# Kernel tuning notes

Hardware: AMD Instinct MI355X
Metric: run time of the kernel (lower is better)

The kernel has to match this reference:

```python
import jax, jax.numpy as jnp
import numpy as np

V, D, H, L, S = 50257, 1024, 16, 4, 4096
DH = D // H  # 64
DF = 4 * D   # 4096


def _layernorm(x, g, b, eps=1e-5):
    m = jnp.mean(x, axis=-1, keepdims=True)
    v = jnp.mean(jnp.square(x - m), axis=-1, keepdims=True)
    return (x - m) / jnp.sqrt(v + eps) * g + b


def _pos_encoding(s, d):
    # standard sinusoidal positional encoding [s, d]
    pos = jnp.arange(s, dtype=jnp.float32)[:, None]
    i = jnp.arange(d // 2, dtype=jnp.float32)[None, :]
    ang = pos * jnp.exp(-(2.0 * i / d) * jnp.log(10000.0))
    return jnp.concatenate([jnp.sin(ang), jnp.cos(ang)], axis=-1)


def setup_inputs() -> dict:
    key = jax.random.key(0)
    ks = jax.random.split(key, 8)
    s = 0.02
    return {
        "tokens": jax.random.randint(ks[0], (S,), 0, V),
        "emb": jax.random.normal(ks[1], (V, D), jnp.float32) * s,
        "Wq": jax.random.normal(ks[2], (L, H, D, DH), jnp.float32) * s,
        "bq": jnp.zeros((L, H, DH), jnp.float32),
        "Wk": jax.random.normal(ks[3], (L, H, D, DH), jnp.float32) * s,
        "bk": jnp.zeros((L, H, DH), jnp.float32),
        "Wv": jax.random.normal(ks[4], (L, H, D, DH), jnp.float32) * s,
        "bv": jnp.zeros((L, H, DH), jnp.float32),
        "ln1_g": jnp.ones((L, D), jnp.float32),
        "ln1_b": jnp.zeros((L, D), jnp.float32),
        "W1": jax.random.normal(ks[5], (L, D, DF), jnp.float32) * s,
        "b1": jnp.zeros((L, DF), jnp.float32),
        "W2": jax.random.normal(ks[6], (L, DF, D), jnp.float32) * s,
        "b2": jnp.zeros((L, D), jnp.float32),
        "ln2_g": jnp.ones((L, D), jnp.float32),
        "ln2_b": jnp.zeros((L, D), jnp.float32),
        "Wout": jax.random.normal(ks[7], (D, V), jnp.float32) * s,
        "bout": jnp.zeros((V,), jnp.float32),
    }


def reference(tokens, emb, Wq, bq, Wk, bk, Wv, bv, ln1_g, ln1_b,
              W1, b1, W2, b2, ln2_g, ln2_b, Wout, bout):
    x = emb[tokens] + _pos_encoding(S, D)          # [S, D]
    scale = 1.0 / jnp.sqrt(jnp.float32(DH))
    for l in range(L):
        # per-head projections: [H, S, DH]
        q = jnp.einsum("sd,hde->hse", x, Wq[l]) + bq[l][:, None, :]
        k = jnp.einsum("sd,hde->hse", x, Wk[l]) + bk[l][:, None, :]
        v = jnp.einsum("sd,hde->hse", x, Wv[l]) + bv[l][:, None, :]
        att = jax.nn.softmax(jnp.einsum("hse,hte->hst", q, k) * scale, axis=-1)
        y = jnp.einsum("hst,hte->hse", att, v)      # [H, S, DH]
        y = jnp.transpose(y, (1, 0, 2)).reshape(S, D)  # concat heads
        x = _layernorm(x + y, ln1_g[l], ln1_b[l])
        y = jnp.maximum(x @ W1[l] + b1[l], 0.0) @ W2[l] + b2[l]  # FFN
        x = _layernorm(x + y, ln2_g[l], ln2_b[l])
    logits = x @ Wout + bout                        # [S, V]
    return jax.nn.softmax(logits, axis=-1)
```

## Files before the change

### kernel.cpp

```cpp
#include <hip/hip_runtime.h>
#include <math.h>

#define S_LEN  4096
#define DMODEL 1024
#define NHEAD  16
#define DHEAD  64
#define DFF    4096
#define NLAYER 4
#define VOCAB  50257
#define NCBP   400

typedef unsigned short ushort_t;
typedef __attribute__((ext_vector_type(8))) __bf16 bf16x8;
typedef __attribute__((ext_vector_type(4))) float f32x4;

static __device__ __forceinline__ ushort_t f2bf(float f) {
  union { float f; unsigned u; } x; x.f = f;
  unsigned r = x.u + 0x7fffu + ((x.u >> 16) & 1u);
  return (ushort_t)(r >> 16);
}
static __device__ __forceinline__ float bf2f(ushort_t h) {
  union { unsigned u; float f; } x; x.u = ((unsigned)h) << 16;
  return x.f;
}
static __device__ __forceinline__ float exp2fast(float x) {
  return __builtin_amdgcn_exp2f(x);
}

#define GLOAD_LDS16(gp, lp) \
  __builtin_amdgcn_global_load_lds((const __attribute__((address_space(1))) void*)(gp), \
                                   (__attribute__((address_space(3))) void*)(lp), 16, 0, 0)

#define QSCALE 0.18033688011112042f

__global__ __launch_bounds__(256) void embed_kernel(
    const int* __restrict__ tokens, const float* __restrict__ emb,
    float* __restrict__ x, ushort_t* __restrict__ xh)
{
  int s = blockIdx.x;
  int tok = tokens[s];
  int d0 = threadIdx.x * 4;
  const double lf = 0.01798894603901598653;
  float4 ev = *(const float4*)(emb + (size_t)tok * DMODEL + d0);
  float o[4]; float evr[4] = {ev.x, ev.y, ev.z, ev.w};
  #pragma unroll
  for (int j = 0; j < 4; ++j) {
    int d = d0 + j;
    int i = (d < 512) ? d : d - 512;
    double ang = (double)s * exp(-lf * (double)i);
    float pe = (d < 512) ? (float)sin(ang) : (float)cos(ang);
    o[j] = evr[j] + pe;
  }
  *(float4*)(x + (size_t)s * DMODEL + d0) = make_float4(o[0], o[1], o[2], o[3]);
  ushort_t hv[4];
  #pragma unroll
  for (int j = 0; j < 4; ++j) hv[j] = f2bf(o[j]);
  *(ushort4*)(xh + (size_t)s * DMODEL + d0) = make_ushort4(hv[0], hv[1], hv[2], hv[3]);
}

__global__ __launch_bounds__(256)
void transpose_split(const float* __restrict__ in, ushort_t* __restrict__ oh,
                     ushort_t* __restrict__ ol,
                     long in_zstr, long out_zoff, long in_z2str, long out_z2off,
                     int zdiv, int in_rstride, int Kout, int Nvalid)
{
  __shared__ float tile[64][65];
  int z1 = blockIdx.z % zdiv, z2 = blockIdx.z / zdiv;
  long ioff = (long)z1 * in_zstr + (long)z2 * in_z2str;
  long ooff = (long)z1 * out_zoff + (long)z2 * out_z2off;
  const float* inz = in + ioff;
  ushort_t* ohz = oh + ooff;
  ushort_t* olz = ol + ooff;
  int k0 = blockIdx.x * 64, n0 = blockIdx.y * 64;
  int t = threadIdx.x;
  #pragma unroll
  for (int i = 0; i < 4; ++i) {
    int idx = t + i * 256;
    int kk = idx >> 4, c4 = idx & 15;
    #pragma unroll
    for (int j = 0; j < 4; ++j) {
      int n = n0 + c4 * 4 + j;
      float v = (n < Nvalid) ? inz[(long)(k0 + kk) * in_rstride + n] : 0.f;
      tile[c4 * 4 + j][kk] = v;
    }
  }
  __syncthreads();
  #pragma unroll
  for (int i = 0; i < 4; ++i) {
    int idx = t + i * 256;
    int nn = idx >> 4, k4 = idx & 15;
    ushort_t hv[4], lv[4];
    #pragma unroll
    for (int j = 0; j < 4; ++j) {
      float v = tile[nn][k4 * 4 + j];
      hv[j] = f2bf(v);
      lv[j] = f2bf(v - bf2f(hv[j]));
    }
    long ob = (long)(n0 + nn) * Kout + k0 + k4 * 4;
    *(ushort4*)(ohz + ob) = make_ushort4(hv[0], hv[1], hv[2], hv[3]);
    *(ushort4*)(olz + ob) = make_ushort4(lv[0], lv[1], lv[2], lv[3]);
  }
}

__global__ __launch_bounds__(256)
void transpose_h(const float* __restrict__ in, ushort_t* __restrict__ oh,
                 int in_rstride, int Kout, int Nvalid)
{
  __shared__ float tile[64][65];
  int k0 = blockIdx.x * 64, n0 = blockIdx.y * 64;
  int t = threadIdx.x;
  #pragma unroll
  for (int i = 0; i < 4; ++i) {
    int idx = t + i * 256;
    int kk = idx >> 4, c4 = idx & 15;
    #pragma unroll
    for (int j = 0; j < 4; ++j) {
      int n = n0 + c4 * 4 + j;
      float v = (n < Nvalid) ? in[(long)(k0 + kk) * in_rstride + n] : 0.f;
      tile[c4 * 4 + j][kk] = v;
    }
  }
  __syncthreads();
  #pragma unroll
  for (int i = 0; i < 4; ++i) {
    int idx = t + i * 256;
    int nn = idx >> 4, k4 = idx & 15;
    ushort_t hv[4];
    #pragma unroll
    for (int j = 0; j < 4; ++j) hv[j] = f2bf(tile[nn][k4 * 4 + j]);
    long ob = (long)(n0 + nn) * Kout + k0 + k4 * 4;
    *(ushort4*)(oh + ob) = make_ushort4(hv[0], hv[1], hv[2], hv[3]);
  }
}

__global__ __launch_bounds__(256)
void transpose_v(const ushort_t* __restrict__ vb, ushort_t* __restrict__ vt)
{
  __shared__ ushort_t tile[64][72];
  int h = blockIdx.y, s0 = blockIdx.x * 64;
  int t = threadIdx.x;
  const ushort_t* src = vb + ((size_t)h * S_LEN + s0) * 64;
  #pragma unroll
  for (int i = 0; i < 4; ++i) {
    int idx = t + i * 256;
    int row = idx >> 4, c4 = idx & 15;
    *(ushort4*)&tile[row][c4 * 4] = *(const ushort4*)(src + (size_t)row * 64 + c4 * 4);
  }
  __syncthreads();
  ushort_t* dst = vt + (size_t)h * DHEAD * S_LEN + s0;
  #pragma unroll
  for (int i = 0; i < 4; ++i) {
    int idx = t + i * 256;
    int e = idx >> 4, s4 = idx & 15;
    ushort4 o = make_ushort4(tile[s4*4+0][e], tile[s4*4+1][e],
                             tile[s4*4+2][e], tile[s4*4+3][e]);
    *(ushort4*)(dst + (size_t)e * S_LEN + s4 * 4) = o;
  }
}

__global__ __launch_bounds__(256)
void concat3_kernel(const float* __restrict__ a, const float* __restrict__ b,
                    const float* __restrict__ c, float* __restrict__ o,
                    int n, long lstrA, long lstrO)
{
  int i = blockIdx.x * 256 + threadIdx.x;
  long l = blockIdx.y;
  if (i < n) {
    o[l * lstrO + i]         = a[l * lstrA + i];
    o[l * lstrO + n + i]     = b[l * lstrA + i];
    o[l * lstrO + 2 * n + i] = c[l * lstrA + i];
  }
}

template<int EPI, bool RELU>
__global__ __launch_bounds__(512, 2)
void gemm8p(const ushort_t* __restrict__ Ah,
            const ushort_t* __restrict__ Bh, const ushort_t* __restrict__ Bl,
            const float* __restrict__ bias, float* __restrict__ C,
            ushort_t* __restrict__ O0, ushort_t* __restrict__ O1,
            ushort_t* __restrict__ O2, ushort_t* __restrict__ O4,
            int K, int ldk, long ldc, long czStride)
{
  constexpr int BUFSTR = 3 * 8192;
  constexpr int OBH = 8192, OBL = 16384;
  __shared__ ushort_t lds[2 * BUFSTR];

  const int t = threadIdx.x;
  const int l = t & 63;
  const int w = t >> 6;
  const int wr = w >> 2;
  const int wc = w & 3;
  const int lrow = l & 15;
  const int lk = (l >> 4) * 8;
  const int l8 = l * 8;
  const long m0 = (long)blockIdx.x * 256;
  const long n0 = (long)blockIdx.y * 256;
  const long kz = (long)blockIdx.z * K;

  const ushort_t *agp[2], *bgp[2], *blgp[2];
  int dst[2];
  #pragma unroll
  for (int i = 0; i < 2; ++i) {
    int s = i * 8 + w;
    dst[i] = s * 512 + l8;
    agp[i]  = Ah + (m0 + s * 16 + lrow) * (long)ldk + kz + lk;
    bgp[i]  = Bh + (n0 + s * 16 + lrow) * (long)ldk + kz + lk;
    blgp[i] = Bl + (n0 + s * 16 + lrow) * (long)ldk + kz + lk;
  }

  f32x4 acc[8][4];
  #pragma unroll
  for (int m = 0; m < 8; ++m)
    #pragma unroll
    for (int n = 0; n < 4; ++n) acc[m][n] = (f32x4)0.f;

  GLOAD_LDS16(agp[0],  &lds[dst[0]]);
  GLOAD_LDS16(agp[1],  &lds[dst[1]]);
  GLOAD_LDS16(bgp[0],  &lds[OBH + dst[0]]);
  GLOAD_LDS16(bgp[1],  &lds[OBH + dst[1]]);
  GLOAD_LDS16(blgp[0], &lds[OBL + dst[0]]);
  GLOAD_LDS16(blgp[1], &lds[OBL + dst[1]]);

  const int nk = K >> 5;
  int cur = 0;
  for (int kt = 0; kt < nk; ++kt) {
    const int knx = (kt + 1 < nk) ? (kt + 1) * 32 : 0;
    ushort_t* cb = &lds[cur * BUFSTR];
    ushort_t* nb = &lds[(cur ^ 1) * BUFSTR];
    bf16x8 af[8], bhf[4], blf[4];

    asm volatile("s_waitcnt vmcnt(2)" ::: "memory");
    __builtin_amdgcn_sched_barrier(0);
    __builtin_amdgcn_s_barrier();
    __builtin_amdgcn_sched_barrier(0);
    #pragma unroll
    for (int m = 0; m < 8; ++m)
      af[m] = *(const bf16x8*)&cb[(wr * 8 + m) * 512 + l8];
    #pragma unroll
    for (int n = 0; n < 4; ++n)
      bhf[n] = *(const bf16x8*)&cb[OBH + (wc * 4 + n) * 512 + l8];
    GLOAD_LDS16(agp[0] + knx, &nb[dst[0]]);
    GLOAD_LDS16(agp[1] + knx, &nb[dst[1]]);
    GLOAD_LDS16(bgp[0] + knx, &nb[OBH + dst[0]]);
    __builtin_amdgcn_s_setprio(1);
    #pragma unroll
    for (int m = 0; m < 8; ++m)
      #pragma unroll
      for (int n = 0; n < 4; ++n)
        acc[m][n] = __builtin_amdgcn_mfma_f32_16x16x32_bf16(af[m], bhf[n], acc[m][n], 0, 0, 0);
    __builtin_amdgcn_s_setprio(0);
    __builtin_amdgcn_sched_barrier(0);

    asm volatile("s_waitcnt vmcnt(3)" ::: "memory");
    __builtin_amdgcn_sched_barrier(0);
    __builtin_amdgcn_s_barrier();
    __builtin_amdgcn_sched_barrier(0);
    #pragma unroll
    for (int n = 0; n < 4; ++n)
      blf[n] = *(const bf16x8*)&cb[OBL + (wc * 4 + n) * 512 + l8];
    GLOAD_LDS16(bgp[1] + knx,  &nb[OBH + dst[1]]);
    GLOAD_LDS16(blgp[0] + knx, &nb[OBL + dst[0]]);
    GLOAD_LDS16(blgp[1] + knx, &nb[OBL + dst[1]]);
    __builtin_amdgcn_s_setprio(1);
    #pragma unroll
    for (int m = 0; m < 8; ++m)
      #pragma unroll
      for (int n = 0; n < 4; ++n)
        acc[m][n] = __builtin_amdgcn_mfma_f32_16x16x32_bf16(af[m], blf[n], acc[m][n], 0, 0, 0);
    __builtin_amdgcn_s_setprio(0);
    __builtin_amdgcn_sched_barrier(0);
    cur ^= 1;
  }
  asm volatile("s_waitcnt vmcnt(0)" ::: "memory");

  if constexpr (EPI == 2) {
    #pragma unroll
    for (int n = 0; n < 4; ++n) {
      long col = n0 + wc * 64 + n * 16 + lrow;
      float bv = bias[col];
      #pragma unroll
      for (int m = 0; m < 8; ++m) {
        #pragma unroll
        for (int r = 0; r < 4; ++r) {
          long row = m0 + wr * 128 + m * 16 + (l >> 4) * 4 + r;
          float v = acc[m][n][r] + bv;
          int c = (int)col;
          if (c < 1024) {
            int hh = c >> 6, e = c & 63;
            float qv = v * QSCALE;
            ushort_t hi = f2bf(qv);
            size_t a = ((size_t)hh * S_LEN + row) * 64 + e;
            O0[a] = hi; O1[a] = f2bf(qv - bf2f(hi));
          } else if (c < 2048) {
            int cc = c - 1024;
            int hh = cc >> 6, e = cc & 63;
            size_t a = ((size_t)hh * S_LEN + row) * 64 + e;
            O2[a] = f2bf(v);
          } else {
            int cc = c - 2048;
            int hh = cc >> 6, e = cc & 63;
            size_t a = ((size_t)hh * S_LEN + row) * 64 + e;
            O4[a] = f2bf(v);
          }
        }
      }
    }
  } else if constexpr (EPI == 1) {
    #pragma unroll
    for (int n = 0; n < 4; ++n) {
      long col = n0 + wc * 64 + n * 16 + lrow;
      float bv = bias[col];
      #pragma unroll
      for (int m = 0; m < 8; ++m) {
        #pragma unroll
        for (int r = 0; r < 4; ++r) {
          long row = m0 + wr * 128 + m * 16 + (l >> 4) * 4 + r;
          float v = acc[m][n][r] + bv;
          if (RELU) v = fmaxf(v, 0.f);
          O0[row * ldc + col] = f2bf(v);
        }
      }
    }
  } else {
    float* Cz = C + (long)blockIdx.z * czStride;
    #pragma unroll
    for (int n = 0; n < 4; ++n) {
      long col = n0 + wc * 64 + n * 16 + lrow;
      #pragma unroll
      for (int m = 0; m < 8; ++m) {
        #pragma unroll
        for (int r = 0; r < 4; ++r) {
          long row = m0 + wr * 128 + m * 16 + (l >> 4) * 4 + r;
          Cz[row * ldc + col] = acc[m][n][r];
        }
      }
    }
  }
}

template<bool BOUND>
__global__ __launch_bounds__(512, 2)
void gemm1p(const ushort_t* __restrict__ Ah, const ushort_t* __restrict__ Bh,
            const float* __restrict__ bias, float* __restrict__ C,
            int K, int ldk, long ldc, int Nlimit,
            float* __restrict__ Ppart, int cbbase)
{
  constexpr int OB = 8192;
  constexpr int BUFSTR = 16384;
  __shared__ ushort_t lds[2 * BUFSTR];
  __shared__ float psum[1024];

  const int t = threadIdx.x;
  const int l = t & 63;
  const int w = t >> 6;
  const int wr = w >> 2;
  const int wc = w & 3;
  const int lrow = l & 15;
  const int lk = (l >> 4) * 8;
  const int l8 = l * 8;
  const long m0 = (long)blockIdx.x * 256;
  const long n0 = (long)blockIdx.y * 256;

  const ushort_t *agp[2], *bgp[2];
  int dst[2];
  #pragma unroll
  for (int i = 0; i < 2; ++i) {
    int s = i * 8 + w;
    dst[i] = s * 512 + l8;
    agp[i] = Ah + (m0 + s * 16 + lrow) * (long)ldk + lk;
    bgp[i] = Bh + (n0 + s * 16 + lrow) * (long)ldk + lk;
  }

  f32x4 acc[8][4];
  #pragma unroll
  for (int m = 0; m < 8; ++m)
    #pragma unroll
    for (int n = 0; n < 4; ++n) acc[m][n] = (f32x4)0.f;

  GLOAD_LDS16(agp[0], &lds[dst[0]]);
  GLOAD_LDS16(agp[1], &lds[dst[1]]);
  GLOAD_LDS16(bgp[0], &lds[OB + dst[0]]);
  GLOAD_LDS16(bgp[1], &lds[OB + dst[1]]);
  GLOAD_LDS16(agp[0] + 32, &lds[BUFSTR + dst[0]]);
  GLOAD_LDS16(agp[1] + 32, &lds[BUFSTR + dst[1]]);
  GLOAD_LDS16(bgp[0] + 32, &lds[BUFSTR + OB + dst[0]]);
  GLOAD_LDS16(bgp[1] + 32, &lds[BUFSTR + OB + dst[1]]);

  const int nk = K >> 5;
  int cur = 0;
  for (int kt = 0; kt < nk; ++kt) {
    ushort_t* cb = &lds[cur * BUFSTR];
    bf16x8 af[8], bhf[4];

    asm volatile("s_waitcnt vmcnt(4)" ::: "memory");
    __builtin_amdgcn_sched_barrier(0);
    __builtin_amdgcn_s_barrier();
    __builtin_amdgcn_sched_barrier(0);
    #pragma unroll
    for (int m = 0; m < 8; ++m)
      af[m] = *(const bf16x8*)&cb[(wr * 8 + m) * 512 + l8];
    #pragma unroll
    for (int n = 0; n < 4; ++n)
      bhf[n] = *(const bf16x8*)&cb[OB + (wc * 4 + n) * 512 + l8];
    __builtin_amdgcn_sched_barrier(0);
    asm volatile("s_waitcnt lgkmcnt(0)" ::: "memory");
    __builtin_amdgcn_sched_barrier(0);
    __builtin_amdgcn_s_barrier();
    __builtin_amdgcn_sched_barrier(0);
    const int knx2 = (kt + 2 < nk) ? (kt + 2) * 32 : 0;
    GLOAD_LDS16(agp[0] + knx2, &cb[dst[0]]);
    GLOAD_LDS16(agp[1] + knx2, &cb[dst[1]]);
    GLOAD_LDS16(bgp[0] + knx2, &cb[OB + dst[0]]);
    GLOAD_LDS16(bgp[1] + knx2, &cb[OB + dst[1]]);
    __builtin_amdgcn_s_setprio(1);
    #pragma unroll
    for (int m = 0; m < 8; ++m)
      #pragma unroll
      for (int n = 0; n < 4; ++n)
        acc[m][n] = __builtin_amdgcn_mfma_f32_16x16x32_bf16(af[m], bhf[n], acc[m][n], 0, 0, 0);
    __builtin_amdgcn_s_setprio(0);
    __builtin_amdgcn_sched_barrier(0);
    cur ^= 1;
  }
  asm volatile("s_waitcnt vmcnt(0)" ::: "memory");

  float smr[8][4];
  #pragma unroll
  for (int m = 0; m < 8; ++m)
    #pragma unroll
    for (int r = 0; r < 4; ++r) smr[m][r] = 0.f;
  #pragma unroll
  for (int n = 0; n < 4; ++n) {
    long col = n0 + wc * 64 + n * 16 + lrow;
    bool cok = (!BOUND) || (col < (long)Nlimit);
    float bv = cok ? bias[col] : 0.f;
    #pragma unroll
    for (int m = 0; m < 8; ++m) {
      #pragma unroll
      for (int r = 0; r < 4; ++r) {
        long row = m0 + wr * 128 + m * 16 + (l >> 4) * 4 + r;
        float e = cok ? __expf(acc[m][n][r] + bv) : 0.f;
        if (cok) C[row * ldc + col] = e;
        smr[m][r] += e;
      }
    }
  }
  #pragma unroll
  for (int m = 0; m < 8; ++m) {
    #pragma unroll
    for (int r = 0; r < 4; ++r) {
      float s = smr[m][r];
      s += __shfl_xor(s, 1);
      s += __shfl_xor(s, 2);
      s += __shfl_xor(s, 4);
      s += __shfl_xor(s, 8);
      if (lrow == 0)
        psum[wc * 256 + wr * 128 + m * 16 + (l >> 4) * 4 + r] = s;
    }
  }
  __syncthreads();
  if (t < 256) {
    float s = psum[t] + psum[256 + t] + psum[512 + t] + psum[768 + t];
    Ppart[(m0 + t) * NCBP + cbbase + blockIdx.y] = s;
  }
}

__global__ __launch_bounds__(256)
void attn_mfma(const ushort_t* __restrict__ qh, const ushort_t* __restrict__ ql,
               const ushort_t* __restrict__ kh, const ushort_t* __restrict__ vt,
               float* __restrict__ y)
{
  __shared__ ushort_t lds[16384];

  const int t = threadIdx.x, l = t & 63, w = t >> 6;
  const int lrow = l & 15, lhi = l >> 4;
  const int h = blockIdx.y;
  const int bw = blockIdx.x * 128 + w * 32;
  const size_t hS = (size_t)h * S_LEN * DHEAD;
  const size_t hV = (size_t)h * DHEAD * S_LEN;
  const int pb = 8192 + w * 2048;

  bf16x8 qhf[2][2], qlf[2][2];
  #pragma unroll
  for (int m = 0; m < 2; ++m)
    #pragma unroll
    for (int ks = 0; ks < 2; ++ks) {
      size_t a = hS + (size_t)(bw + m * 16 + lrow) * 64 + ks * 32 + lhi * 8;
      qhf[m][ks] = *(const bf16x8*)(qh + a);
      qlf[m][ks] = *(const bf16x8*)(ql + a);
    }

  f32x4 acc[2][4];
  #pragma unroll
  for (int m = 0; m < 2; ++m)
    #pragma unroll
    for (int n = 0; n < 4; ++n) acc[m][n] = (f32x4)0.f;
  float mrow[8], lsum[8];
  #pragma unroll
  for (int i = 0; i < 8; ++i) { mrow[i] = -1e30f; lsum[i] = 0.f; }

  for (int kt = 0; kt < S_LEN; kt += 64) {
    __syncthreads();
    #pragma unroll
    for (int i = 0; i < 2; ++i) {
      int s = i * 4 + w;
      size_t krow = (size_t)(kt + (s >> 1) * 16 + lrow);
      int koff = (s & 1) * 32 + lhi * 8;
      GLOAD_LDS16(kh + hS + krow * 64 + koff, &lds[s * 512 + l * 8]);
      size_t erow = (size_t)((s >> 1) * 16 + lrow);
      int toff = kt + (s & 1) * 32 + lhi * 8;
      GLOAD_LDS16(vt + hV + erow * S_LEN + toff, &lds[4096 + s * 512 + l * 8]);
    }
    __syncthreads();

    f32x4 sacc[2][4];
    #pragma unroll
    for (int m = 0; m < 2; ++m)
      #pragma unroll
      for (int n = 0; n < 4; ++n) sacc[m][n] = (f32x4)0.f;
    #pragma unroll
    for (int ks = 0; ks < 2; ++ks) {
      bf16x8 bh_[4];
      #pragma unroll
      for (int n = 0; n < 4; ++n)
        bh_[n] = *(const bf16x8*)&lds[(n * 2 + ks) * 512 + l * 8];
      #pragma unroll
      for (int m = 0; m < 2; ++m)
        #pragma unroll
        for (int n = 0; n < 4; ++n) {
          sacc[m][n] = __builtin_amdgcn_mfma_f32_16x16x32_bf16(qhf[m][ks], bh_[n], sacc[m][n], 0, 0, 0);
          sacc[m][n] = __builtin_amdgcn_mfma_f32_16x16x32_bf16(qlf[m][ks], bh_[n], sacc[m][n], 0, 0, 0);
        }
    }

    float tmv[2][4];
    bool up = false;
    #pragma unroll
    for (int m = 0; m < 2; ++m) {
      #pragma unroll
      for (int r = 0; r < 4; ++r) {
        float tm = fmaxf(fmaxf(sacc[m][0][r], sacc[m][1][r]),
                         fmaxf(sacc[m][2][r], sacc[m][3][r]));
        tm = fmaxf(tm, __shfl_xor(tm, 1));
        tm = fmaxf(tm, __shfl_xor(tm, 2));
        tm = fmaxf(tm, __shfl_xor(tm, 4));
        tm = fmaxf(tm, __shfl_xor(tm, 8));
        tmv[m][r] = tm;
        up = up || (tm > mrow[m * 4 + r]);
      }
    }
    if (__ballot(up) != 0ULL) {
      #pragma unroll
      for (int m = 0; m < 2; ++m) {
        #pragma unroll
        for (int r = 0; r < 4; ++r) {
          const int idx = m * 4 + r;
          float mn = fmaxf(mrow[idx], tmv[m][r]);
          float al = exp2fast(mrow[idx] - mn);
          mrow[idx] = mn;
          lsum[idx] *= al;
          #pragma unroll
          for (int n = 0; n < 4; ++n) acc[m][n][r] *= al;
        }
      }
    }
    #pragma unroll
    for (int m = 0; m < 2; ++m) {
      #pragma unroll
      for (int r = 0; r < 4; ++r) {
        const int idx = m * 4 + r;
        float rs = 0.f;
        #pragma unroll
        for (int n = 0; n < 4; ++n) {
          float p = exp2fast(sacc[m][n][r] - mrow[idx]);
          rs += p;
          int pa = pb + ((m * 2 + (n >> 1)) << 9) + (((n & 1) * 2 + (lrow >> 3)) << 7)
                   + ((lhi * 4 + r) << 3) + (l & 7);
          pa ^= (lrow >> 3) << 3;
          lds[pa] = f2bf(p);
        }
        rs += __shfl_xor(rs, 1);
        rs += __shfl_xor(rs, 2);
        rs += __shfl_xor(rs, 4);
        rs += __shfl_xor(rs, 8);
        lsum[idx] += rs;
      }
    }

    #pragma unroll
    for (int ks = 0; ks < 2; ++ks) {
      bf16x8 pa_[2];
      #pragma unroll
      for (int m = 0; m < 2; ++m) {
        int ra = pb + ((m * 2 + ks) << 9) + (l << 3);
        ra ^= ((l >> 4) & 1) << 3;
        pa_[m] = *(const bf16x8*)&lds[ra];
      }
      #pragma unroll
      for (int n = 0; n < 4; ++n) {
        bf16x8 vf = *(const bf16x8*)&lds[4096 + (n * 2 + ks) * 512 + l * 8];
        #pragma unroll
        for (int m = 0; m < 2; ++m)
          acc[m][n] = __builtin_amdgcn_mfma_f32_16x16x32_bf16(pa_[m], vf, acc[m][n], 0, 0, 0);
      }
    }
  }

  #pragma unroll
  for (int m = 0; m < 2; ++m) {
    #pragma unroll
    for (int r = 0; r < 4; ++r) {
      float inv = 1.0f / lsum[m * 4 + r];
      int row = bw + m * 16 + lhi * 4 + r;
      #pragma unroll
      for (int n = 0; n < 4; ++n)
        y[(size_t)row * DMODEL + h * 64 + n * 16 + lrow] = acc[m][n][r] * inv;
    }
  }
}

__device__ __forceinline__ float block_sum256(float v, float* sm)
{
  #pragma unroll
  for (int off = 32; off >= 1; off >>= 1) v += __shfl_xor(v, off);
  int w = threadIdx.x >> 6;
  if ((threadIdx.x & 63) == 0) sm[w] = v;
  __syncthreads();
  v = sm[0] + sm[1] + sm[2] + sm[3];
  __syncthreads();
  return v;
}

__global__ __launch_bounds__(256)
void resid_ln_kernel(float* __restrict__ x, const float* __restrict__ y,
                     const float* __restrict__ g, const float* __restrict__ b,
                     ushort_t* __restrict__ xh)
{
  __shared__ float sm[4];
  int row = blockIdx.x, t = threadIdx.x;
  float4 xv = *(const float4*)(x + (size_t)row * DMODEL + t * 4);
  float4 yv = *(const float4*)(y + (size_t)row * DMODEL + t * 4);
  float a0 = xv.x + yv.x, a1 = xv.y + yv.y, a2 = xv.z + yv.z, a3 = xv.w + yv.w;
  float s = block_sum256(a0 + a1 + a2 + a3, sm);
  float mean = s * (1.0f / DMODEL);
  float d0 = a0 - mean, d1 = a1 - mean, d2 = a2 - mean, d3 = a3 - mean;
  float vs = block_sum256(d0*d0 + d1*d1 + d2*d2 + d3*d3, sm);
  float inv = rsqrtf(vs * (1.0f / DMODEL) + 1e-5f);
  float4 gv = *(const float4*)(g + t * 4);
  float4 bv = *(const float4*)(b + t * 4);
  float o[4];
  o[0] = d0 * inv * gv.x + bv.x;
  o[1] = d1 * inv * gv.y + bv.y;
  o[2] = d2 * inv * gv.z + bv.z;
  o[3] = d3 * inv * gv.w + bv.w;
  *(float4*)(x + (size_t)row * DMODEL + t * 4) = make_float4(o[0], o[1], o[2], o[3]);
  ushort_t hv[4];
  #pragma unroll
  for (int j = 0; j < 4; ++j) hv[j] = f2bf(o[j]);
  *(ushort4*)(xh + (size_t)row * DMODEL + t * 4) = make_ushort4(hv[0], hv[1], hv[2], hv[3]);
}

__global__ __launch_bounds__(256)
void resid_ln_red(float* __restrict__ x, const float* __restrict__ parts,
                  long pstride, const float* __restrict__ bias,
                  const float* __restrict__ g, const float* __restrict__ b,
                  ushort_t* __restrict__ xh)
{
  __shared__ float sm[4];
  int row = blockIdx.x, t = threadIdx.x;
  size_t base = (size_t)row * DMODEL + t * 4;
  float4 xv = *(const float4*)(x + base);
  float4 bb = *(const float4*)(bias + t * 4);
  float a0 = xv.x + bb.x, a1 = xv.y + bb.y, a2 = xv.z + bb.z, a3 = xv.w + bb.w;
  #pragma unroll
  for (int z = 0; z < 4; ++z) {
    float4 pv = *(const float4*)(parts + (size_t)z * pstride + base);
    a0 += pv.x; a1 += pv.y; a2 += pv.z; a3 += pv.w;
  }
  float s = block_sum256(a0 + a1 + a2 + a3, sm);
  float mean = s * (1.0f / DMODEL);
  float d0 = a0 - mean, d1 = a1 - mean, d2 = a2 - mean, d3 = a3 - mean;
  float vs = block_sum256(d0*d0 + d1*d1 + d2*d2 + d3*d3, sm);
  float inv = rsqrtf(vs * (1.0f / DMODEL) + 1e-5f);
  float4 gv = *(const float4*)(g + t * 4);
  float4 bv = *(const float4*)(b + t * 4);
  float o[4];
  o[0] = d0 * inv * gv.x + bv.x;
  o[1] = d1 * inv * gv.y + bv.y;
  o[2] = d2 * inv * gv.z + bv.z;
  o[3] = d3 * inv * gv.w + bv.w;
  *(float4*)(x + base) = make_float4(o[0], o[1], o[2], o[3]);
  ushort_t hv[4];
  #pragma unroll
  for (int j = 0; j < 4; ++j) hv[j] = f2bf(o[j]);
  *(ushort4*)(xh + base) = make_ushort4(hv[0], hv[1], hv[2], hv[3]);
}

__global__ __launch_bounds__(256)
void scale_softmax(float* __restrict__ out, const float* __restrict__ partials,
                   int ncb)
{
  __shared__ float sm[4];
  int row = blockIdx.x, t = threadIdx.x;
  float s = 0.f;
  for (int cb = t; cb < ncb; cb += 256) s += partials[(size_t)row * NCBP + cb];
  s = block_sum256(s, sm);
  float inv = 1.0f / s;
  float* p = out + (size_t)row * VOCAB;
  int head = (int)((((uintptr_t)16 - ((uintptr_t)p & 15)) & 15) >> 2);
  if (t < head) p[t] *= inv;
  int nvec = (VOCAB - head) >> 2;
  float4* pv = (float4*)(p + head);
  for (int i = t; i < nvec; i += 256) {
    float4 v = pv[i];
    v.x *= inv; v.y *= inv; v.z *= inv; v.w *= inv;
    pv[i] = v;
  }
  int done = head + nvec * 4;
  if (t < VOCAB - done) p[done + t] *= inv;
}

extern "C" void kernel_launch(void* const* d_in, const int* in_sizes, int n_in,
                              void* d_out, int out_size, void* d_ws, size_t ws_size,
                              hipStream_t stream)
{
  const int*   tokens = (const int*)  d_in[0];
  const float* emb    = (const float*)d_in[1];
  const float* Wq     = (const float*)d_in[2];
  const float* bq     = (const float*)d_in[3];
  const float* Wk     = (const float*)d_in[4];
  const float* bk     = (const float*)d_in[5];
  const float* Wv     = (const float*)d_in[6];
  const float* bv     = (const float*)d_in[7];
  const float* ln1g   = (const float*)d_in[8];
  const float* ln1b   = (const float*)d_in[9];
  const float* W1     = (const float*)d_in[10];
  const float* b1     = (const float*)d_in[11];
  const float* W2     = (const float*)d_in[12];
  const float* b2     = (const float*)d_in[13];
  const float* ln2g   = (const float*)d_in[14];
  const float* ln2b   = (const float*)d_in[15];
  const float* Wout   = (const float*)d_in[16];
  const float* bout   = (const float*)d_in[17];

  char* wsb = (char*)d_ws;
  ushort_t* xh     = (ushort_t*)(wsb);
  ushort_t* stripH = (ushort_t*)(wsb + ((size_t)8  << 20));
  float*    partials = (float*)(wsb + ((size_t)24 << 20));

  char* ob = (char*)d_out;
  float*    x     = (float*)(ob);
  float*    yb    = (float*)(ob + ((size_t)16  << 20));
  ushort_t* qh    = (ushort_t*)(ob + ((size_t)32  << 20));
  ushort_t* ql    = (ushort_t*)(ob + ((size_t)40  << 20));
  ushort_t* kh    = (ushort_t*)(ob + ((size_t)48  << 20));
  ushort_t* vb16  = (ushort_t*)(ob + ((size_t)56  << 20));
  ushort_t* vt    = (ushort_t*)(ob + ((size_t)64  << 20));
  ushort_t* h1h   = (ushort_t*)(ob + ((size_t)72  << 20));
  float*    fparts= (float*)(ob + ((size_t)104 << 20));
  ushort_t* wqkvhA= (ushort_t*)(ob + ((size_t)168 << 20));
  ushort_t* wqkvlA= (ushort_t*)(ob + ((size_t)192 << 20));
  ushort_t* w1hA  = (ushort_t*)(ob + ((size_t)216 << 20));
  ushort_t* w1lA  = (ushort_t*)(ob + ((size_t)248 << 20));
  ushort_t* w2hA  = (ushort_t*)(ob + ((size_t)280 << 20));
  ushort_t* w2lA  = (ushort_t*)(ob + ((size_t)312 << 20));
  float*    bqkvA = (float*)(ob + ((size_t)344 << 20));
  float*    outf  = (float*)d_out;

  const long WQKV_L = 3072L * 1024;
  const long WFF_L  = 4096L * 1024;

  embed_kernel<<<S_LEN, 256, 0, stream>>>(tokens, emb, x, xh);

  transpose_split<<<dim3(16, 1, 64), 256, 0, stream>>>(
      Wq, wqkvhA, wqkvlA,
      (long)DMODEL * DHEAD, (long)DHEAD * DMODEL,
      (long)NHEAD * DMODEL * DHEAD, WQKV_L,
      16, DHEAD, DMODEL, DHEAD);
  transpose_split<<<dim3(16, 1, 64), 256, 0, stream>>>(
      Wk, wqkvhA + 1024 * 1024, wqkvlA + 1024 * 1024,
      (long)DMODEL * DHEAD, (long)DHEAD * DMODEL,
      (long)NHEAD * DMODEL * DHEAD, WQKV_L,
      16, DHEAD, DMODEL, DHEAD);
  transpose_split<<<dim3(16, 1, 64), 256, 0, stream>>>(
      Wv, wqkvhA + 2048 * 1024, wqkvlA + 2048 * 1024,
      (long)DMODEL * DHEAD, (long)DHEAD * DMODEL,
      (long)NHEAD * DMODEL * DHEAD, WQKV_L,
      16, DHEAD, DMODEL, DHEAD);
  transpose_split<<<dim3(16, 64, 4), 256, 0, stream>>>(
      W1, w1hA, w1lA, 0, 0,
      (long)DMODEL * DFF, WFF_L, 1, DFF, DMODEL, DFF);
  transpose_split<<<dim3(64, 16, 4), 256, 0, stream>>>(
      W2, w2hA, w2lA, 0, 0,
      (long)DFF * DMODEL, WFF_L, 1, DMODEL, DFF, DMODEL);
  concat3_kernel<<<dim3(4, NLAYER), 256, 0, stream>>>(
      bq, bk, bv, bqkvA, 1024, 1024, 3072);

  for (int l = 0; l < NLAYER; ++l) {
    const ushort_t* wqh = wqkvhA + (long)l * WQKV_L;
    const ushort_t* wql = wqkvlA + (long)l * WQKV_L;
    const ushort_t* w1h = w1hA + (long)l * WFF_L;
    const ushort_t* w1l = w1lA + (long)l * WFF_L;
    const ushort_t* w2h = w2hA + (long)l * WFF_L;
    const ushort_t* w2l = w2lA + (long)l * WFF_L;

    gemm8p<2, false><<<dim3(16, 12), 512, 0, stream>>>(
        xh, wqh, wql, bqkvA + (long)l * 3072, nullptr,
        qh, ql, kh, vb16, 1024, 1024, 0, 0);
    transpose_v<<<dim3(64, 16), 256, 0, stream>>>(vb16, vt);

    attn_mfma<<<dim3(32, 16), 256, 0, stream>>>(qh, ql, kh, vt, yb);

    resid_ln_kernel<<<S_LEN, 256, 0, stream>>>(x, yb,
        ln1g + (size_t)l * DMODEL, ln1b + (size_t)l * DMODEL, xh);

    gemm8p<1, true><<<dim3(16, 16), 512, 0, stream>>>(
        xh, w1h, w1l, b1 + (long)l * DFF, nullptr,
        h1h, nullptr, nullptr, nullptr, 1024, 1024, 4096, 0);
    gemm8p<0, false><<<dim3(16, 4, 4), 512, 0, stream>>>(
        h1h, w2h, w2l, nullptr, fparts,
        nullptr, nullptr, nullptr, nullptr,
        1024, 4096, 1024, (long)S_LEN * DMODEL);
    resid_ln_red<<<S_LEN, 256, 0, stream>>>(x, fparts, (long)S_LEN * DMODEL,
        b2 + (long)l * DMODEL,
        ln2g + (size_t)l * DMODEL, ln2b + (size_t)l * DMODEL, xh);
  }

  const int SW = 4096;
  for (int is = 0; is < 12; ++is) {
    int n0 = is * SW;
    transpose_h<<<dim3(16, 64, 1), 256, 0, stream>>>(
        Wout + n0, stripH, VOCAB, DMODEL, SW);
    gemm1p<false><<<dim3(16, 16), 512, 0, stream>>>(
        xh, stripH, bout + n0, outf + n0,
        1024, 1024, VOCAB, SW, partials, is * 16);
  }
  {
    int n0 = 12 * SW;
    int ncols = VOCAB - n0;
    int nt64 = (ncols + 63) / 64;
    int nb256 = (ncols + 255) / 256;
    transpose_h<<<dim3(16, nt64, 1), 256, 0, stream>>>(
        Wout + n0, stripH, VOCAB, DMODEL, ncols);
    gemm1p<true><<<dim3(16, nb256), 512, 0, stream>>>(
        xh, stripH, bout + n0, outf + n0,
        1024, 1024, VOCAB, ncols, partials, 12 * 16);
  }
  const int ncb = (VOCAB + 255) / 256;
  scale_softmax<<<S_LEN, 256, 0, stream>>>(outf, partials, ncb);
}
```

Before: 3.820 ms.

## Double-buffer attention K/V loads, fuse V transpose into QKV epilogue, single-shot vocab GEMM

The attention kernel now double-buffers its K/V tiles in LDS, prefetching the next tile while the current one is computed, with a single barrier per iteration. The QKV GEMM epilogue writes V directly in transposed layout, which removes the separate transpose_v kernel and one round trip through memory. When the workspace is large enough, the output projection transposes all of Wout once and runs one GEMM over the whole vocabulary instead of twelve strip launches. The costs are more LDS per block, strided scattered stores in the V epilogue, and a dependence on workspace size.

```diff
diff --git a/kernel.cpp b/kernel.cpp
--- a/kernel.cpp
+++ b/kernel.cpp
@@ -130,31 +130,6 @@
     for (int j = 0; j < 4; ++j) hv[j] = f2bf(tile[nn][k4 * 4 + j]);
     long ob = (long)(n0 + nn) * Kout + k0 + k4 * 4;
     *(ushort4*)(oh + ob) = make_ushort4(hv[0], hv[1], hv[2], hv[3]);
-  }
-}
-
-__global__ __launch_bounds__(256)
-void transpose_v(const ushort_t* __restrict__ vb, ushort_t* __restrict__ vt)
-{
-  __shared__ ushort_t tile[64][72];
-  int h = blockIdx.y, s0 = blockIdx.x * 64;
-  int t = threadIdx.x;
-  const ushort_t* src = vb + ((size_t)h * S_LEN + s0) * 64;
-  #pragma unroll
-  for (int i = 0; i < 4; ++i) {
-    int idx = t + i * 256;
-    int row = idx >> 4, c4 = idx & 15;
-    *(ushort4*)&tile[row][c4 * 4] = *(const ushort4*)(src + (size_t)row * 64 + c4 * 4);
-  }
-  __syncthreads();
-  ushort_t* dst = vt + (size_t)h * DHEAD * S_LEN + s0;
-  #pragma unroll
-  for (int i = 0; i < 4; ++i) {
-    int idx = t + i * 256;
-    int e = idx >> 4, s4 = idx & 15;
-    ushort4 o = make_ushort4(tile[s4*4+0][e], tile[s4*4+1][e],
-                             tile[s4*4+2][e], tile[s4*4+3][e]);
-    *(ushort4*)(dst + (size_t)e * S_LEN + s4 * 4) = o;
   }
 }
 
@@ -299,7 +274,7 @@
           } else {
             int cc = c - 2048;
             int hh = cc >> 6, e = cc & 63;
-            size_t a = ((size_t)hh * S_LEN + row) * 64 + e;
+            size_t a = ((size_t)hh * DHEAD + e) * S_LEN + row;
             O4[a] = f2bf(v);
           }
         }
@@ -470,7 +445,7 @@
                const ushort_t* __restrict__ kh, const ushort_t* __restrict__ vt,
                float* __restrict__ y)
 {
-  __shared__ ushort_t lds[16384];
+  __shared__ ushort_t lds[24576];
 
   const int t = threadIdx.x, l = t & 63, w = t >> 6;
   const int lrow = l & 15, lhi = l >> 4;
@@ -478,7 +453,7 @@
   const int bw = blockIdx.x * 128 + w * 32;
   const size_t hS = (size_t)h * S_LEN * DHEAD;
   const size_t hV = (size_t)h * DHEAD * S_LEN;
-  const int pb = 8192 + w * 2048;
+  const int pb = 16384 + w * 2048;
 
   bf16x8 qhf[2][2], qlf[2][2];
   #pragma unroll
@@ -499,19 +474,37 @@
   #pragma unroll
   for (int i = 0; i < 8; ++i) { mrow[i] = -1e30f; lsum[i] = 0.f; }
 
+  #pragma unroll
+  for (int i = 0; i < 2; ++i) {
+    int s = i * 4 + w;
+    size_t krow = (size_t)((s >> 1) * 16 + lrow);
+    int koff = (s & 1) * 32 + lhi * 8;
+    GLOAD_LDS16(kh + hS + krow * 64 + koff, &lds[s * 512 + l * 8]);
+    int toff = (s & 1) * 32 + lhi * 8;
+    GLOAD_LDS16(vt + hV + krow * S_LEN + toff, &lds[4096 + s * 512 + l * 8]);
+  }
+
+  int cur = 0;
   for (int kt = 0; kt < S_LEN; kt += 64) {
-    __syncthreads();
-    #pragma unroll
-    for (int i = 0; i < 2; ++i) {
-      int s = i * 4 + w;
-      size_t krow = (size_t)(kt + (s >> 1) * 16 + lrow);
-      int koff = (s & 1) * 32 + lhi * 8;
-      GLOAD_LDS16(kh + hS + krow * 64 + koff, &lds[s * 512 + l * 8]);
-      size_t erow = (size_t)((s >> 1) * 16 + lrow);
-      int toff = kt + (s & 1) * 32 + lhi * 8;
-      GLOAD_LDS16(vt + hV + erow * S_LEN + toff, &lds[4096 + s * 512 + l * 8]);
-    }
-    __syncthreads();
+    asm volatile("s_waitcnt vmcnt(0)" ::: "memory");
+    __builtin_amdgcn_sched_barrier(0);
+    __builtin_amdgcn_s_barrier();
+    __builtin_amdgcn_sched_barrier(0);
+    ushort_t* cb = &lds[cur * 8192];
+    if (kt + 64 < S_LEN) {
+      ushort_t* nb = &lds[(cur ^ 1) * 8192];
+      int kn = kt + 64;
+      #pragma unroll
+      for (int i = 0; i < 2; ++i) {
+        int s = i * 4 + w;
+        size_t krow = (size_t)(kn + (s >> 1) * 16 + lrow);
+        int koff = (s & 1) * 32 + lhi * 8;
+        GLOAD_LDS16(kh + hS + krow * 64 + koff, &nb[s * 512 + l * 8]);
+        size_t erow = (size_t)((s >> 1) * 16 + lrow);
+        int toff = kn + (s & 1) * 32 + lhi * 8;
+        GLOAD_LDS16(vt + hV + erow * S_LEN + toff, &nb[4096 + s * 512 + l * 8]);
+      }
+    }
 
     f32x4 sacc[2][4];
     #pragma unroll
@@ -523,7 +516,7 @@
       bf16x8 bh_[4];
       #pragma unroll
       for (int n = 0; n < 4; ++n)
-        bh_[n] = *(const bf16x8*)&lds[(n * 2 + ks) * 512 + l * 8];
+        bh_[n] = *(const bf16x8*)&cb[(n * 2 + ks) * 512 + l * 8];
       #pragma unroll
       for (int m = 0; m < 2; ++m)
         #pragma unroll
@@ -598,12 +591,13 @@
       }
       #pragma unroll
       for (int n = 0; n < 4; ++n) {
-        bf16x8 vf = *(const bf16x8*)&lds[4096 + (n * 2 + ks) * 512 + l * 8];
+        bf16x8 vf = *(const bf16x8*)&cb[4096 + (n * 2 + ks) * 512 + l * 8];
         #pragma unroll
         for (int m = 0; m < 2; ++m)
           acc[m][n] = __builtin_amdgcn_mfma_f32_16x16x32_bf16(pa_[m], vf, acc[m][n], 0, 0, 0);
       }
     }
+    cur ^= 1;
   }
 
   #pragma unroll
@@ -747,6 +741,8 @@
   ushort_t* xh     = (ushort_t*)(wsb);
   ushort_t* stripH = (ushort_t*)(wsb + ((size_t)8  << 20));
   float*    partials = (float*)(wsb + ((size_t)24 << 20));
+  ushort_t* woutT  = (ushort_t*)(wsb + ((size_t)32 << 20));
+  const bool bigws = ws_size >= ((size_t)137 << 20);
 
   char* ob = (char*)d_out;
   float*    x     = (float*)(ob);
@@ -754,17 +750,16 @@
   ushort_t* qh    = (ushort_t*)(ob + ((size_t)32  << 20));
   ushort_t* ql    = (ushort_t*)(ob + ((size_t)40  << 20));
   ushort_t* kh    = (ushort_t*)(ob + ((size_t)48  << 20));
-  ushort_t* vb16  = (ushort_t*)(ob + ((size_t)56  << 20));
-  ushort_t* vt    = (ushort_t*)(ob + ((size_t)64  << 20));
-  ushort_t* h1h   = (ushort_t*)(ob + ((size_t)72  << 20));
-  float*    fparts= (float*)(ob + ((size_t)104 << 20));
-  ushort_t* wqkvhA= (ushort_t*)(ob + ((size_t)168 << 20));
-  ushort_t* wqkvlA= (ushort_t*)(ob + ((size_t)192 << 20));
-  ushort_t* w1hA  = (ushort_t*)(ob + ((size_t)216 << 20));
-  ushort_t* w1lA  = (ushort_t*)(ob + ((size_t)248 << 20));
-  ushort_t* w2hA  = (ushort_t*)(ob + ((size_t)280 << 20));
-  ushort_t* w2lA  = (ushort_t*)(ob + ((size_t)312 << 20));
-  float*    bqkvA = (float*)(ob + ((size_t)344 << 20));
+  ushort_t* vt    = (ushort_t*)(ob + ((size_t)56  << 20));
+  ushort_t* h1h   = (ushort_t*)(ob + ((size_t)64  << 20));
+  float*    fparts= (float*)(ob + ((size_t)96  << 20));
+  ushort_t* wqkvhA= (ushort_t*)(ob + ((size_t)160 << 20));
+  ushort_t* wqkvlA= (ushort_t*)(ob + ((size_t)184 << 20));
+  ushort_t* w1hA  = (ushort_t*)(ob + ((size_t)208 << 20));
+  ushort_t* w1lA  = (ushort_t*)(ob + ((size_t)240 << 20));
+  ushort_t* w2hA  = (ushort_t*)(ob + ((size_t)272 << 20));
+  ushort_t* w2lA  = (ushort_t*)(ob + ((size_t)304 << 20));
+  float*    bqkvA = (float*)(ob + ((size_t)336 << 20));
   float*    outf  = (float*)d_out;
 
   const long WQKV_L = 3072L * 1024;
@@ -806,8 +801,7 @@
 
     gemm8p<2, false><<<dim3(16, 12), 512, 0, stream>>>(
         xh, wqh, wql, bqkvA + (long)l * 3072, nullptr,
-        qh, ql, kh, vb16, 1024, 1024, 0, 0);
-    transpose_v<<<dim3(64, 16), 256, 0, stream>>>(vb16, vt);
+        qh, ql, kh, vt, 1024, 1024, 0, 0);
 
     attn_mfma<<<dim3(32, 16), 256, 0, stream>>>(qh, ql, kh, vt, yb);
 
@@ -826,16 +820,21 @@
         ln2g + (size_t)l * DMODEL, ln2b + (size_t)l * DMODEL, xh);
   }
 
-  const int SW = 4096;
-  for (int is = 0; is < 12; ++is) {
-    int n0 = is * SW;
-    transpose_h<<<dim3(16, 64, 1), 256, 0, stream>>>(
-        Wout + n0, stripH, VOCAB, DMODEL, SW);
-    gemm1p<false><<<dim3(16, 16), 512, 0, stream>>>(
-        xh, stripH, bout + n0, outf + n0,
-        1024, 1024, VOCAB, SW, partials, is * 16);
-  }
-  {
+  if (bigws) {
+    transpose_h<<<dim3(16, 786, 1), 256, 0, stream>>>(
+        Wout, woutT, VOCAB, DMODEL, VOCAB);
+    gemm1p<true><<<dim3(16, 197), 512, 0, stream>>>(
+        xh, woutT, bout, outf, 1024, 1024, VOCAB, VOCAB, partials, 0);
+  } else {
+    const int SW = 4096;
+    for (int is = 0; is < 12; ++is) {
+      int n0 = is * SW;
+      transpose_h<<<dim3(16, 64, 1), 256, 0, stream>>>(
+          Wout + n0, stripH, VOCAB, DMODEL, SW);
+      gemm1p<false><<<dim3(16, 16), 512, 0, stream>>>(
+          xh, stripH, bout + n0, outf + n0,
+          1024, 1024, VOCAB, SW, partials, is * 16);
+    }
     int n0 = 12 * SW;
     int ncols = VOCAB - n0;
     int nt64 = (ncols + 63) / 64;
```

Result: faster. 3.704 ms (-3.0%).
